# Performance work log

Hardware: AMD Instinct MI355X
Metric: run time of the kernel (lower is better)

The kernel has to match this reference:

```python
import jax, jax.numpy as jnp
import numpy as np

# Dimensions (Gemma-2B-like, uniform q-head rank)
B, S, HID = 2, 2048, 2048
H, HKV, D = 16, 8, 128
RQ, RK, RV = 64, 64, 64
G = H // HKV  # heads per kv group
SCALE = D ** -0.5
NEG_INF = -1e9


def setup_inputs() -> dict:
    key = jax.random.key(0)
    ks = jax.random.split(key, 9)
    hidden_states = jax.random.normal(ks[0], (B, S, HID), dtype=jnp.float32)
    W_A_q = jax.random.normal(ks[1], (H * RQ, HID), dtype=jnp.float32) * 0.02
    W_A_k = jax.random.normal(ks[2], (HKV * RK, HID), dtype=jnp.float32) * 0.02
    W_A_v = jax.random.normal(ks[3], (HKV * RV, HID), dtype=jnp.float32) * 0.02
    B_q = jax.random.normal(ks[4], (H, RQ, D), dtype=jnp.float32)
    B_k = jax.random.normal(ks[5], (HKV, RK, D), dtype=jnp.float32)
    B_v = jax.random.normal(ks[6], (HKV, RV, D), dtype=jnp.float32)
    W_o = jax.random.normal(ks[7], (HID, H * D), dtype=jnp.float32) * 0.02
    # RoPE tables (cos/sin form of gemma's complex freqs_cis)
    inv_freq = 1.0 / (10000.0 ** (jnp.arange(0, D, 2, dtype=jnp.float32) / D))
    freqs = jnp.arange(S, dtype=jnp.float32)[:, None] * inv_freq[None, :]  # [S, D/2]
    freqs_cos = jnp.cos(freqs)
    freqs_sin = jnp.sin(freqs)
    # Causal additive mask [1, 1, S, S]
    causal = jnp.tril(jnp.ones((S, S), dtype=bool))
    mask = jnp.where(causal, 0.0, NEG_INF).astype(jnp.float32)[None, None]
    kv_write_indices = jnp.arange(S, dtype=jnp.int32)
    return {
        'hidden_states': hidden_states, 'W_A_q': W_A_q, 'W_A_k': W_A_k,
        'W_A_v': W_A_v, 'B_q': B_q, 'B_k': B_k, 'B_v': B_v, 'W_o': W_o,
        'freqs_cos': freqs_cos, 'freqs_sin': freqs_sin, 'mask': mask,
        'kv_write_indices': kv_write_indices,
    }


def _rope(x, cos, sin):
    # x: [b, s, h, d]; gemma pairs first half with second half of head_dim
    x1, x2 = jnp.split(x, 2, axis=-1)
    c = cos[None, :, None, :]
    s = sin[None, :, None, :]
    return jnp.concatenate([x1 * c - x2 * s, x1 * s + x2 * c], axis=-1)


def reference(hidden_states, W_A_q, W_A_k, W_A_v, B_q, B_k, B_v, W_o,
              freqs_cos, freqs_sin, mask, kv_write_indices):
    b, s, _ = hidden_states.shape
    # Low-rank A factors
    A_q = jnp.einsum('bsd,rd->bsr', hidden_states, W_A_q).reshape(b, s, H, RQ)
    A_k = jnp.einsum('bsd,rd->bsr', hidden_states, W_A_k).reshape(b, s, HKV, RK)
    A_v = jnp.einsum('bsd,rd->bsr', hidden_states, W_A_v).reshape(b, s, HKV, RV)
    # Factorized KV cache: scatter A factors at write indices (prefill)
    cache_kA = jnp.zeros((b, s, HKV, RK), hidden_states.dtype).at[:, kv_write_indices].set(A_k)
    cache_vA = jnp.zeros((b, s, HKV, RV), hidden_states.dtype).at[:, kv_write_indices].set(A_v)
    # GQA expansion of cached A factors
    gidx = jnp.repeat(jnp.arange(HKV), G)  # [H]
    A_k_rep = cache_kA[:, :, gidx]  # [b, kv, H, RK]
    A_v_rep = cache_vA[:, :, gidx]
    # Reconstruct Q/K/V from constant B factors (per-head loop vectorized:
    # all q ranks equal, so einsum over heads is the same math)
    q = jnp.einsum('bshr,hrd->bshd', A_q, B_q) / RQ
    k = jnp.einsum('bkhr,hrd->bkhd', A_k_rep, B_k[gidx]) / RK
    v = jnp.einsum('bkhr,hrd->bkhd', A_v_rep, B_v[gidx]) / RV
    # RoPE post-reconstruction
    q = _rope(q, freqs_cos, freqs_sin)
    k = _rope(k, freqs_cos, freqs_sin)
    # Attention
    scores = jnp.einsum('bqhd,bkhd->bhqk', q, k) * SCALE + mask
    probs = jax.nn.softmax(scores, axis=-1)
    out = jnp.einsum('bhqk,bkhd->bqhd', probs, v).reshape(b, s, H * D)
    return jnp.einsum('bse,he->bsh', out, W_o)
```

## Files before the change

### kernel.cpp

```cpp
#include <hip/hip_runtime.h>
#include <hip/hip_bf16.h>

typedef __attribute__((ext_vector_type(8))) short bf16x8;
typedef __attribute__((ext_vector_type(4))) float f32x4;

#define MFMA_16x16x32(a,b,c) __builtin_amdgcn_mfma_f32_16x16x32_bf16((a),(b),(c),0,0,0)

__device__ __forceinline__ unsigned short f2b(float f){
  unsigned int u = __builtin_bit_cast(unsigned int, f);
  u = u + 0x7FFFu + ((u >> 16) & 1u);
  return (unsigned short)(u >> 16);
}
__device__ __forceinline__ float b2f(unsigned short h){
  unsigned int u = ((unsigned int)h) << 16;
  return __builtin_bit_cast(float, u);
}

__device__ __forceinline__ void gload_lds16(const unsigned short* g, unsigned short* l){
  __builtin_amdgcn_global_load_lds(
      (const __attribute__((address_space(1))) void*)g,
      (__attribute__((address_space(3))) void*)l, 16, 0, 0);
}


__global__ void cvt_f32_bf16(const float* __restrict__ src, unsigned short* __restrict__ dst, int n4){
  int i = blockIdx.x * blockDim.x + threadIdx.x;
  int stride = gridDim.x * blockDim.x;
  for (; i < n4; i += stride){
    float4 v = reinterpret_cast<const float4*>(src)[i];
    ushort4 o;
    o.x = f2b(v.x); o.y = f2b(v.y); o.z = f2b(v.z); o.w = f2b(v.w);
    reinterpret_cast<ushort4*>(dst)[i] = o;
  }
}

__global__ void cvt_factor_t(const float* __restrict__ src, unsigned short* __restrict__ dst, int n){
  int i = blockIdx.x * blockDim.x + threadIdx.x;
  if (i >= n) return;
  int d = i & 127, r = (i >> 7) & 63, h = i >> 13;
  dst[(h << 13) + (d << 6) + r] = f2b(src[i]);
}

__global__ void rope_inplace(unsigned short* __restrict__ buf,
                             const float* __restrict__ fc,
                             const float* __restrict__ fs, int total){
  int i = blockIdx.x * blockDim.x + threadIdx.x;
  if (i >= total) return;
  int d4 = (i & 15) << 2;
  int s  = (i >> 4) & 2047;
  size_t base = ((size_t)(i >> 4)) * 128;
  ushort4 x1 = *reinterpret_cast<ushort4*>(buf + base + d4);
  ushort4 x2 = *reinterpret_cast<ushort4*>(buf + base + 64 + d4);
  float4 c  = *reinterpret_cast<const float4*>(fc + (size_t)s*64 + d4);
  float4 sn = *reinterpret_cast<const float4*>(fs + (size_t)s*64 + d4);
  ushort4 o1, o2; float a, b;
  a = b2f(x1.x); b = b2f(x2.x); o1.x = f2b(a*c.x - b*sn.x); o2.x = f2b(a*sn.x + b*c.x);
  a = b2f(x1.y); b = b2f(x2.y); o1.y = f2b(a*c.y - b*sn.y); o2.y = f2b(a*sn.y + b*c.y);
  a = b2f(x1.z); b = b2f(x2.z); o1.z = f2b(a*c.z - b*sn.z); o2.z = f2b(a*sn.z + b*c.z);
  a = b2f(x1.w); b = b2f(x2.w); o1.w = f2b(a*c.w - b*sn.w); o2.w = f2b(a*sn.w + b*c.w);
  *reinterpret_cast<ushort4*>(buf + base + d4)      = o1;
  *reinterpret_cast<ushort4*>(buf + base + 64 + d4) = o2;
}


template<int OUT_F32>
__global__ __launch_bounds__(256) void gemm_bt(
    const unsigned short* __restrict__ A, const unsigned short* __restrict__ B,
    void* __restrict__ Cv, int N, int K, float scale)
{
  __shared__ unsigned short As[128*64];
  __shared__ unsigned short Bs[128*64];
  const int tid = threadIdx.x;
  const int mb = blockIdx.x, nb = blockIdx.y;
  const int w = tid >> 6, lane = tid & 63;
  const int wr = w >> 1, wc = w & 1;
  const int l16 = lane & 15, lg = lane >> 4;

  f32x4 acc[4][4] = {};

  const int srow = tid >> 3;
  const int scol = (tid & 7) << 3;

  const unsigned short* Ap = A + (size_t)(mb*128)*K;
  const unsigned short* Bp = B + (size_t)(nb*128)*K;

  bf16x8 ar[4], br[4];
  #pragma unroll
  for (int c = 0; c < 4; c++){
    ar[c] = *reinterpret_cast<const bf16x8*>(Ap + (size_t)(srow + 32*c)*K + scol);
    br[c] = *reinterpret_cast<const bf16x8*>(Bp + (size_t)(srow + 32*c)*K + scol);
  }
  const int nkt = K >> 6;
  for (int kt = 0; kt < nkt; kt++){
    __syncthreads();
    #pragma unroll
    for (int c = 0; c < 4; c++){
      int r = srow + 32*c;
      int idx = (r*64 + scol) ^ ((r & 7) << 3);
      *reinterpret_cast<bf16x8*>(&As[idx]) = ar[c];
      *reinterpret_cast<bf16x8*>(&Bs[idx]) = br[c];
    }
    __syncthreads();
    if (kt + 1 < nkt){
      const unsigned short* Ap2 = Ap + (size_t)(kt+1)*64;
      const unsigned short* Bp2 = Bp + (size_t)(kt+1)*64;
      #pragma unroll
      for (int c = 0; c < 4; c++){
        ar[c] = *reinterpret_cast<const bf16x8*>(Ap2 + (size_t)(srow + 32*c)*K + scol);
        br[c] = *reinterpret_cast<const bf16x8*>(Bp2 + (size_t)(srow + 32*c)*K + scol);
      }
    }
    #pragma unroll
    for (int t = 0; t < 2; t++){
      bf16x8 af[4], bf[4];
      #pragma unroll
      for (int i = 0; i < 4; i++){
        int rowA = wr*64 + i*16 + l16;
        int col  = t*32 + lg*8;
        af[i] = *reinterpret_cast<const bf16x8*>(&As[(rowA*64 + col) ^ ((rowA & 7) << 3)]);
        int rowB = wc*64 + i*16 + l16;
        bf[i] = *reinterpret_cast<const bf16x8*>(&Bs[(rowB*64 + col) ^ ((rowB & 7) << 3)]);
      }
      #pragma unroll
      for (int i = 0; i < 4; i++)
        #pragma unroll
        for (int j = 0; j < 4; j++)
          acc[i][j] = MFMA_16x16x32(af[i], bf[j], acc[i][j]);
    }
  }
  #pragma unroll
  for (int i = 0; i < 4; i++){
    #pragma unroll
    for (int j = 0; j < 4; j++){
      int row = mb*128 + wr*64 + i*16 + lg*4;
      int col = nb*128 + wc*64 + j*16 + l16;
      #pragma unroll
      for (int r = 0; r < 4; r++){
        float v = acc[i][j][r] * scale;
        if (OUT_F32) reinterpret_cast<float*>(Cv)[(size_t)(row + r)*N + col] = v;
        else reinterpret_cast<unsigned short*>(Cv)[(size_t)(row + r)*N + col] = f2b(v);
      }
    }
  }
}


__global__ __launch_bounds__(256) void factor_gemm(
    const unsigned short* __restrict__ A,
    const unsigned short* __restrict__ Bt,
    unsigned short* __restrict__ Out, int coloff, int Hn, float scale)
{
  __shared__ unsigned short As[128*64];
  __shared__ unsigned short Bs[128*64];
  const int tid = threadIdx.x;
  const int mb = blockIdx.x;
  const int h  = blockIdx.y;
  const int w = tid >> 6, lane = tid & 63;
  const int wr = w >> 1, wc = w & 1;
  const int l16 = lane & 15, lg = lane >> 4;

  const int srow = tid >> 3;
  const int scol = (tid & 7) << 3;

  const unsigned short* Ap = A + (size_t)(mb*128)*2048 + coloff + h*64;
  const unsigned short* Bp = Bt + (size_t)h*(128*64);

  #pragma unroll
  for (int c = 0; c < 4; c++){
    int r = srow + 32*c;
    int idx = (r*64 + scol) ^ ((r & 7) << 3);
    *reinterpret_cast<bf16x8*>(&As[idx]) = *reinterpret_cast<const bf16x8*>(Ap + (size_t)r*2048 + scol);
    *reinterpret_cast<bf16x8*>(&Bs[idx]) = *reinterpret_cast<const bf16x8*>(Bp + r*64 + scol);
  }
  __syncthreads();

  f32x4 acc[4][4] = {};
  #pragma unroll
  for (int t = 0; t < 2; t++){
    bf16x8 af[4], bf[4];
    #pragma unroll
    for (int i = 0; i < 4; i++){
      int rowA = wr*64 + i*16 + l16;
      int col  = t*32 + lg*8;
      af[i] = *reinterpret_cast<const bf16x8*>(&As[(rowA*64 + col) ^ ((rowA & 7) << 3)]);
      int rowB = wc*64 + i*16 + l16;
      bf[i] = *reinterpret_cast<const bf16x8*>(&Bs[(rowB*64 + col) ^ ((rowB & 7) << 3)]);
    }
    #pragma unroll
    for (int i = 0; i < 4; i++)
      #pragma unroll
      for (int j = 0; j < 4; j++)
        acc[i][j] = MFMA_16x16x32(af[i], bf[j], acc[i][j]);
  }

  #pragma unroll
  for (int i = 0; i < 4; i++){
    #pragma unroll
    for (int j = 0; j < 4; j++){
      int row0 = mb*128 + wr*64 + i*16 + lg*4;
      int d    = wc*64 + j*16 + l16;
      #pragma unroll
      for (int r = 0; r < 4; r++){
        int row = row0 + r;
        int b = row >> 11, s = row & 2047;
        Out[((size_t)(b*Hn + h)*2048 + s)*128 + d] = f2b(acc[i][j][r] * scale);
      }
    }
  }
}


__device__ __forceinline__ int vt_idx(int d, int kv){
  return d*64 + ((((kv >> 3) + d + (d >> 3)) & 7) << 3) + (kv & 7);
}

__global__ __launch_bounds__(256) void flash_attn(
    const unsigned short* __restrict__ Q,
    const unsigned short* __restrict__ Kb,
    const unsigned short* __restrict__ Vb,
    unsigned short* __restrict__ O)
{
  __shared__ unsigned short Ks[64*128];
  __shared__ unsigned short Vrow[64*128];
  __shared__ unsigned short Vt[128*64];
  __shared__ unsigned short Pl[4][16*64];

  const int tid = threadIdx.x;
  const int w = tid >> 6, lane = tid & 63;
  const int l16 = lane & 15, lg = lane >> 4;
  const int h = blockIdx.y, b = blockIdx.z;
  const int hkv = h >> 1;

  const size_t hbase  = ((size_t)(b*16 + h))*2048*128;
  const size_t kvbase = ((size_t)(b*8 + hkv))*2048*128;

  const int sR = w*16 + (lane >> 4);
  const int sC = (lane & 15) * 8;

  auto stage = [&](int kb){
    #pragma unroll
    for (int i = 0; i < 4; i++){
      int R = sR + i*4;
      const unsigned short* gk = Kb + kvbase + (size_t)(kb*64 + R)*128 + (sC ^ ((R & 7) << 3));
      gload_lds16(gk, &Ks[(w*16 + i*4)*128]);
      const unsigned short* gv = Vb + kvbase + (size_t)(kb*64 + R)*128 + sC;
      gload_lds16(gv, &Vrow[(w*16 + i*4)*128]);
    }
  };

  stage(0);
  __syncthreads();

  const int tkv0 = (tid >> 4) * 4;
  const int td0  = (tid & 15) * 8;

  const int qtiles[2] = { (int)blockIdx.x, 31 - (int)blockIdx.x };

  for (int ph = 0; ph < 2; ph++){
    const int qe = qtiles[ph];
    const size_t qbase = hbase + (size_t)(qe*64 + w*16)*128;
    const int qrow0 = qe*64 + w*16 + lg*4;

    bf16x8 aq[4];
    #pragma unroll
    for (int t = 0; t < 4; t++)
      aq[t] = *reinterpret_cast<const bf16x8*>(&Q[qbase + (size_t)l16*128 + t*32 + lg*8]);

    f32x4 oac[8] = {};
    float mrow[4], lrow[4];
    #pragma unroll
    for (int r = 0; r < 4; r++){ mrow[r] = -1e30f; lrow[r] = 0.f; }

    for (int kb = 0; kb <= qe; kb++){
      bf16x8 vr0 = *reinterpret_cast<const bf16x8*>(&Vrow[(tkv0 + 0)*128 + td0]);
      bf16x8 vr1 = *reinterpret_cast<const bf16x8*>(&Vrow[(tkv0 + 1)*128 + td0]);
      bf16x8 vr2 = *reinterpret_cast<const bf16x8*>(&Vrow[(tkv0 + 2)*128 + td0]);
      bf16x8 vr3 = *reinterpret_cast<const bf16x8*>(&Vrow[(tkv0 + 3)*128 + td0]);

      f32x4 sac[4] = {};
      #pragma unroll
      for (int nt = 0; nt < 4; nt++){
        #pragma unroll
        for (int t = 0; t < 4; t++){
          int rowK = nt*16 + l16;
          int col  = t*32 + lg*8;
          bf16x8 bk = *reinterpret_cast<const bf16x8*>(&Ks[(rowK*128 + col) ^ ((rowK & 7) << 3)]);
          sac[nt] = MFMA_16x16x32(aq[t], bk, sac[nt]);
        }
      }

      #pragma unroll
      for (int j = 0; j < 8; j++){
        unsigned int lo = (unsigned int)(unsigned short)vr0[j] | ((unsigned int)(unsigned short)vr1[j] << 16);
        unsigned int hi = (unsigned int)(unsigned short)vr2[j] | ((unsigned int)(unsigned short)vr3[j] << 16);
        uint2 u; u.x = lo; u.y = hi;
        *reinterpret_cast<uint2*>(&Vt[vt_idx(td0 + j, tkv0)]) = u;
      }

      if (kb == qe){
        #pragma unroll
        for (int nt = 0; nt < 4; nt++){
          int kcol = kb*64 + nt*16 + l16;
          #pragma unroll
          for (int r = 0; r < 4; r++)
            if (kcol > qrow0 + r) sac[nt][r] = -1e30f;
        }
      }
      float corr[4];
      #pragma unroll
      for (int r = 0; r < 4; r++){
        float v = fmaxf(fmaxf(sac[0][r], sac[1][r]), fmaxf(sac[2][r], sac[3][r]));
        v = fmaxf(v, __shfl_xor(v, 1));
        v = fmaxf(v, __shfl_xor(v, 2));
        v = fmaxf(v, __shfl_xor(v, 4));
        v = fmaxf(v, __shfl_xor(v, 8));
        float mn = fmaxf(mrow[r], v);
        corr[r] = __expf(mrow[r] - mn);
        mrow[r] = mn;
      }
      float rs[4] = {0.f, 0.f, 0.f, 0.f};
      #pragma unroll
      for (int nt = 0; nt < 4; nt++){
        #pragma unroll
        for (int r = 0; r < 4; r++){
          float p = __expf(sac[nt][r] - mrow[r]);
          sac[nt][r] = p;
          rs[r] += p;
        }
      }
      #pragma unroll
      for (int r = 0; r < 4; r++){
        float v = rs[r];
        v += __shfl_xor(v, 1); v += __shfl_xor(v, 2); v += __shfl_xor(v, 4); v += __shfl_xor(v, 8);
        lrow[r] = lrow[r]*corr[r] + v;
      }
      #pragma unroll
      for (int dn = 0; dn < 8; dn++)
        #pragma unroll
        for (int r = 0; r < 4; r++) oac[dn][r] *= corr[r];

      #pragma unroll
      for (int nt = 0; nt < 4; nt++){
        #pragma unroll
        for (int r = 0; r < 4; r++){
          int row = lg*4 + r, col = nt*16 + l16;
          Pl[w][(row*64 + col) ^ ((row & 7) << 3)] = f2b(sac[nt][r]);
        }
      }

      __syncthreads();
      if (kb < qe) stage(kb + 1);
      else if (ph == 0) stage(0);

      #pragma unroll
      for (int t = 0; t < 2; t++){
        int colp = t*32 + lg*8;
        bf16x8 ap = *reinterpret_cast<const bf16x8*>(&Pl[w][(l16*64 + colp) ^ ((l16 & 7) << 3)]);
        #pragma unroll
        for (int dn = 0; dn < 8; dn++){
          int rowV = dn*16 + l16;
          bf16x8 bv = *reinterpret_cast<const bf16x8*>(&Vt[vt_idx(rowV, colp)]);
          oac[dn] = MFMA_16x16x32(ap, bv, oac[dn]);
        }
      }
      __syncthreads();
    }

    #pragma unroll
    for (int dn = 0; dn < 8; dn++){
      #pragma unroll
      for (int r = 0; r < 4; r++){
        int row = qe*64 + w*16 + lg*4 + r;
        O[((size_t)(b*2048 + row))*2048 + h*128 + dn*16 + l16] = f2b(oac[dn][r] / lrow[r]);
      }
    }
  }
}


extern "C" void kernel_launch(void* const* d_in, const int* in_sizes, int n_in,
                              void* d_out, int out_size, void* d_ws, size_t ws_size,
                              hipStream_t stream)
{
  if (n_in < 10) return;
  const float* hidden = (const float*)d_in[0];
  const float* WAq = (const float*)d_in[1];
  const float* WAk = (const float*)d_in[2];
  const float* WAv = (const float*)d_in[3];
  const float* Bq  = (const float*)d_in[4];
  const float* Bk  = (const float*)d_in[5];
  const float* Bv  = (const float*)d_in[6];
  const float* Wo  = (const float*)d_in[7];
  const float* fcos = (const float*)d_in[8];
  const float* fsin = (const float*)d_in[9];
  float* out = (float*)d_out;

  char* p = (char*)d_ws;
  auto take = [&](size_t bytes){ char* q = p; p += (bytes + 255) & ~(size_t)255; return q; };
  unsigned short* Xb   = (unsigned short*)take((size_t)4096*2048*2);
  unsigned short* Wqkv = (unsigned short*)take((size_t)2048*2048*2);
  unsigned short* Wob  = (unsigned short*)take((size_t)2048*2048*2);
  unsigned short* Aqkv = (unsigned short*)take((size_t)4096*2048*2);
  unsigned short* Bqt  = (unsigned short*)take((size_t)16*128*64*2);
  unsigned short* Bkt  = (unsigned short*)take((size_t)8*128*64*2);
  unsigned short* Bvt  = (unsigned short*)take((size_t)8*128*64*2);
  unsigned short* qbuf = (unsigned short*)take((size_t)2*16*2048*128*2);
  unsigned short* kbuf = (unsigned short*)take((size_t)2*8*2048*128*2);
  unsigned short* vbuf = (unsigned short*)take((size_t)2*8*2048*128*2);
  unsigned short* aout = (unsigned short*)take((size_t)4096*2048*2);
  if ((size_t)(p - (char*)d_ws) > ws_size) return;

  auto cvt = [&](const float* s, unsigned short* d, size_t n){
    int n4 = (int)(n >> 2);
    int blocks = (n4 + 255) / 256; if (blocks > 4096) blocks = 4096;
    cvt_f32_bf16<<<blocks, 256, 0, stream>>>(s, d, n4);
  };
  cvt(hidden, Xb, (size_t)4096*2048);
  cvt(WAq, Wqkv,                       (size_t)1024*2048);
  cvt(WAk, Wqkv + (size_t)1024*2048,   (size_t)512*2048);
  cvt(WAv, Wqkv + (size_t)1536*2048,   (size_t)512*2048);
  cvt(Wo,  Wob, (size_t)2048*2048);
  cvt_factor_t<<<(16*64*128)/256, 256, 0, stream>>>(Bq, Bqt, 16*64*128);
  cvt_factor_t<<<(8*64*128)/256, 256, 0, stream>>>(Bk, Bkt, 8*64*128);
  cvt_factor_t<<<(8*64*128)/256, 256, 0, stream>>>(Bv, Bvt, 8*64*128);

  gemm_bt<0><<<dim3(32,16), 256, 0, stream>>>(Xb, Wqkv, (void*)Aqkv, 2048, 2048, 1.0f);

  const float SCALE = 0.08838834764831845f;
  factor_gemm<<<dim3(32,16), 256, 0, stream>>>(Aqkv, Bqt, qbuf, 0,    16, SCALE/64.0f);
  factor_gemm<<<dim3(32,8),  256, 0, stream>>>(Aqkv, Bkt, kbuf, 1024, 8,  1.0f/64.0f);
  factor_gemm<<<dim3(32,8),  256, 0, stream>>>(Aqkv, Bvt, vbuf, 1536, 8,  1.0f/64.0f);

  rope_inplace<<<(32*2048*16)/256, 256, 0, stream>>>(qbuf, fcos, fsin, 32*2048*16);
  rope_inplace<<<(16*2048*16)/256, 256, 0, stream>>>(kbuf, fcos, fsin, 16*2048*16);

  flash_attn<<<dim3(16,16,2), 256, 0, stream>>>(qbuf, kbuf, vbuf, aout);

  gemm_bt<1><<<dim3(32,16), 256, 0, stream>>>(aout, Wob, (void*)out, 2048, 2048, 1.0f);
}
```

Before: 391.7 us.

## Double-buffer gemm_bt LDS tiles with direct global-to-LDS async loads

```diff
diff --git a/kernel.cpp b/kernel.cpp
--- a/kernel.cpp
+++ b/kernel.cpp
@@ -68,8 +68,8 @@
     const unsigned short* __restrict__ A, const unsigned short* __restrict__ B,
     void* __restrict__ Cv, int N, int K, float scale)
 {
-  __shared__ unsigned short As[128*64];
-  __shared__ unsigned short Bs[128*64];
+  __shared__ unsigned short As[2][128*64];
+  __shared__ unsigned short Bs[2][128*64];
   const int tid = threadIdx.x;
   const int mb = blockIdx.x, nb = blockIdx.y;
   const int w = tid >> 6, lane = tid & 63;
@@ -78,38 +78,31 @@
 
   f32x4 acc[4][4] = {};
 
-  const int srow = tid >> 3;
-  const int scol = (tid & 7) << 3;
-
   const unsigned short* Ap = A + (size_t)(mb*128)*K;
   const unsigned short* Bp = B + (size_t)(nb*128)*K;
 
-  bf16x8 ar[4], br[4];
-  #pragma unroll
-  for (int c = 0; c < 4; c++){
-    ar[c] = *reinterpret_cast<const bf16x8*>(Ap + (size_t)(srow + 32*c)*K + scol);
-    br[c] = *reinterpret_cast<const bf16x8*>(Bp + (size_t)(srow + 32*c)*K + scol);
-  }
+  const int sRo = 32*w + (lane >> 3);
+  const int sCo = ((lane & 7) ^ (lane >> 3)) << 3;
+  const int ldsW = 2048*w;
+
+  auto stage = [&](int kt, int buf){
+    const unsigned short* Ak = Ap + (size_t)kt*64 + sCo;
+    const unsigned short* Bk = Bp + (size_t)kt*64 + sCo;
+    #pragma unroll
+    for (int i = 0; i < 4; i++)
+      gload_lds16(Ak + (size_t)(sRo + 8*i)*K, &As[buf][ldsW + 512*i]);
+    #pragma unroll
+    for (int i = 0; i < 4; i++)
+      gload_lds16(Bk + (size_t)(sRo + 8*i)*K, &Bs[buf][ldsW + 512*i]);
+  };
+
   const int nkt = K >> 6;
+  stage(0, 0);
+  __syncthreads();
+
+  int cur = 0;
   for (int kt = 0; kt < nkt; kt++){
-    __syncthreads();
-    #pragma unroll
-    for (int c = 0; c < 4; c++){
-      int r = srow + 32*c;
-      int idx = (r*64 + scol) ^ ((r & 7) << 3);
-      *reinterpret_cast<bf16x8*>(&As[idx]) = ar[c];
-      *reinterpret_cast<bf16x8*>(&Bs[idx]) = br[c];
-    }
-    __syncthreads();
-    if (kt + 1 < nkt){
-      const unsigned short* Ap2 = Ap + (size_t)(kt+1)*64;
-      const unsigned short* Bp2 = Bp + (size_t)(kt+1)*64;
-      #pragma unroll
-      for (int c = 0; c < 4; c++){
-        ar[c] = *reinterpret_cast<const bf16x8*>(Ap2 + (size_t)(srow + 32*c)*K + scol);
-        br[c] = *reinterpret_cast<const bf16x8*>(Bp2 + (size_t)(srow + 32*c)*K + scol);
-      }
-    }
+    if (kt + 1 < nkt) stage(kt + 1, cur ^ 1);
     #pragma unroll
     for (int t = 0; t < 2; t++){
       bf16x8 af[4], bf[4];
@@ -117,9 +110,9 @@
       for (int i = 0; i < 4; i++){
         int rowA = wr*64 + i*16 + l16;
         int col  = t*32 + lg*8;
-        af[i] = *reinterpret_cast<const bf16x8*>(&As[(rowA*64 + col) ^ ((rowA & 7) << 3)]);
+        af[i] = *reinterpret_cast<const bf16x8*>(&As[cur][(rowA*64 + col) ^ ((rowA & 7) << 3)]);
         int rowB = wc*64 + i*16 + l16;
-        bf[i] = *reinterpret_cast<const bf16x8*>(&Bs[(rowB*64 + col) ^ ((rowB & 7) << 3)]);
+        bf[i] = *reinterpret_cast<const bf16x8*>(&Bs[cur][(rowB*64 + col) ^ ((rowB & 7) << 3)]);
       }
       #pragma unroll
       for (int i = 0; i < 4; i++)
@@ -127,7 +120,10 @@
         for (int j = 0; j < 4; j++)
           acc[i][j] = MFMA_16x16x32(af[i], bf[j], acc[i][j]);
     }
-  }
+    __syncthreads();
+    cur ^= 1;
+  }
+
   #pragma unroll
   for (int i = 0; i < 4; i++){
     #pragma unroll
```

Measured after the change: 384.7 us. No clear change (-1.8%).
